# Optimization experiments

Measured on AMD Instinct MI355X. Metric: run time of the kernel, lower is better.

Reference implementation:

```python
import jax, jax.numpy as jnp
import numpy as np

B, IN_CH, HID, OUT_CH, GH, GW = 16, 64, 128, 64, 64, 64


def grid_edges(h, w):
    # torch_geometric.utils.grid: 8-neighborhood + self-loop, edge = (node, node+offset)
    idx = np.arange(h * w).reshape(h, w)
    rows, cols = [], []
    for dr in (-1, 0, 1):
        for dc in (-1, 0, 1):
            node = idx[max(0, -dr):h - max(0, dr), max(0, -dc):w - max(0, dc)]
            nb = idx[max(0, dr):h + min(0, dr) or None, max(0, dc):w + min(0, dc) or None]
            rows.append(node.ravel())
            cols.append(nb.ravel())
    return np.stack([np.concatenate(rows), np.concatenate(cols)])


def setup_inputs() -> dict:
    key = jax.random.key(0)
    ks = jax.random.split(key, 32)
    def rn(i, shape, scale=0.05):
        return jax.random.normal(ks[i], shape, dtype=jnp.float32) * scale
    e = grid_edges(GH, GW)                                   # (2, E)
    offs = (np.arange(B) * (GH * GW)).reshape(B, 1, 1)
    ei = (e[None] + offs).transpose(1, 0, 2).reshape(2, -1)  # (2, B*E) batched offsets
    return {
        "x": rn(0, (B, IN_CH, GH, GW), 1.0),
        "cW1": rn(1, (HID, IN_CH, 3, 3)), "cb1": rn(2, (HID,)),
        "cW2": rn(3, (IN_CH, HID, 3, 3)), "cb2": rn(4, (IN_CH,)),
        "q1W": rn(5, (HID, IN_CH)), "q1b": rn(6, (HID,)),
        "k1W": rn(7, (HID, IN_CH)), "k1b": rn(8, (HID,)),
        "v1W": rn(9, (HID, IN_CH)), "v1b": rn(10, (HID,)),
        "s1W": rn(11, (HID, IN_CH)), "s1b": rn(12, (HID,)),
        "q2W": rn(13, (IN_CH, HID)), "q2b": rn(14, (IN_CH,)),
        "k2W": rn(15, (IN_CH, HID)), "k2b": rn(16, (IN_CH,)),
        "v2W": rn(17, (IN_CH, HID)), "v2b": rn(18, (IN_CH,)),
        "s2W": rn(19, (IN_CH, HID)), "s2b": rn(20, (IN_CH,)),
        "fW1": rn(21, (HID, 2 * IN_CH, 3, 3)), "fb1": rn(22, (HID,)),
        "fW2": rn(23, (OUT_CH, HID, 3, 3)), "fb2": rn(24, (OUT_CH,)),
        "edge_index": jnp.asarray(ei, dtype=jnp.int32),
    }


def gelu(x):
    return jax.nn.gelu(x, approximate=False)


def sn_conv(x, W, b):
    # spectral_norm: power iteration on (O, I*k*k) matrix; u,v detached, grad through sigma
    O = W.shape[0]
    Wm = W.reshape(O, -1)
    u = jnp.ones((O,), W.dtype) / jnp.sqrt(jnp.asarray(O, W.dtype))
    for _ in range(3):
        v = Wm.T @ u
        v = v / (jnp.linalg.norm(v) + 1e-12)
        u = Wm @ v
        u = u / (jnp.linalg.norm(u) + 1e-12)
    u = jax.lax.stop_gradient(u)
    v = jax.lax.stop_gradient(v)
    sigma = u @ (Wm @ v)
    Wn = W / sigma
    xp = jnp.pad(x, ((0, 0), (0, 0), (1, 1), (1, 1)), mode='edge')  # replicate padding
    y = jax.lax.conv_general_dilated(xp, Wn, (1, 1), 'VALID',
                                     dimension_numbers=('NCHW', 'OIHW', 'NCHW'))
    return y + b[None, :, None, None]


def tconv(x, src, dst, N, heads, qW, qb, kW, kb, vW, vb, sW, sb):
    # PyG TransformerConv (concat=True, root_weight=True, no edge features)
    d = qW.shape[0] // heads
    q = (x @ qW.T + qb)[dst].reshape(-1, heads, d)
    k = (x @ kW.T + kb)[src].reshape(-1, heads, d)
    v = (x @ vW.T + vb)[src].reshape(-1, heads, d)
    alpha = (q * k).sum(-1) / jnp.sqrt(jnp.asarray(d, x.dtype))      # (E, heads)
    m = jax.ops.segment_max(alpha, dst, num_segments=N)               # scatter-softmax
    a = jnp.exp(alpha - m[dst])
    s = jax.ops.segment_sum(a, dst, num_segments=N)
    a = a / (s[dst] + 1e-16)
    out = jax.ops.segment_sum(a[:, :, None] * v, dst, num_segments=N)  # (N, heads, d)
    return out.reshape(N, heads * d) + x @ sW.T + sb


def reference(x, cW1, cb1, cW2, cb2, q1W, q1b, k1W, k1b, v1W, v1b, s1W, s1b,
              q2W, q2b, k2W, k2b, v2W, v2b, s2W, s2b, fW1, fb1, fW2, fb2, edge_index):
    Bb, C, Hc, Wc = x.shape
    N = Bb * Hc * Wc
    # CNN branch (DoubleConvBlock)
    x1 = gelu(sn_conv(gelu(sn_conv(x, cW1, cb1)), cW2, cb2))
    # GCN branch
    xf = x.transpose(0, 2, 3, 1).reshape(N, C)
    src, dst = edge_index[0], edge_index[1]
    h = gelu(tconv(xf, src, dst, N, 8, q1W, q1b, k1W, k1b, v1W, v1b, s1W, s1b))
    h = gelu(tconv(h, src, dst, N, 1, q2W, q2b, k2W, k2b, v2W, v2b, s2W, s2b))
    x2 = h.reshape(Bb, Hc, Wc, -1).transpose(0, 3, 1, 2)
    # Fusion
    xc = jnp.concatenate([x1, x2], axis=1)
    return gelu(sn_conv(gelu(sn_conv(xc, fW1, fb1)), fW2, fb2))
```

## Files before the change

kernel.cpp:

```cpp
#include <hip/hip_runtime.h>
#include <hip/hip_bf16.h>

typedef unsigned int  u32;
typedef unsigned short u16;
typedef __attribute__((ext_vector_type(8))) short bf16x8;
typedef __attribute__((ext_vector_type(4))) float f32x4;
typedef __attribute__((ext_vector_type(4))) u32 u32x4;

#define NPIX 65536

constexpr size_t SIG   = 0;
constexpr size_t B1OFF = 256;
constexpr size_t B2OFF = B1OFF + 2048;
constexpr size_t WC1   = B2OFF + 1024;
constexpr size_t WC2   = WC1 + 147456;
constexpr size_t WF1   = WC2 + 147456;
constexpr size_t WF2   = WF1 + 294912;
constexpr size_t WP1   = WF2 + 147456;
constexpr size_t WP2   = WP1 + 65536;
constexpr size_t XB    = WP2 + 65536;
constexpr size_t HBUF  = XB + 8388608;
constexpr size_t QKVS2 = HBUF + 16777216;
constexpr size_t XC    = QKVS2 + 33554432;
constexpr size_t QKVS1 = XC + 16777216;
constexpr size_t Y1    = QKVS1;
constexpr size_t TBUF  = QKVS1 + 16777216;
constexpr size_t GRAM  = QKVS1 + 67108864;

__device__ __forceinline__ float gelu_f(float v) {
    float xa = fabsf(v) * 0.70710678118654752f;
    float t  = __fdividef(1.0f, fmaf(0.3275911f, xa, 1.0f));
    float poly = t * fmaf(t, fmaf(t, fmaf(t, fmaf(t, 1.061405429f, -1.453152027f),
                   1.421413741f), -0.284496736f), 0.254829592f);
    float erfv = 1.0f - poly * __expf(-xa * xa);
    erfv = copysignf(erfv, v);
    return 0.5f * v * (1.0f + erfv);
}
__device__ __forceinline__ u16 f2bf(float f) {
    __hip_bfloat16 b = __float2bfloat16(f);
    return *reinterpret_cast<u16*>(&b);
}
__device__ __forceinline__ float blo(u32 u) {
    union { u32 i; float f; } x; x.i = u << 16; return x.f;
}
__device__ __forceinline__ float bhi(u32 u) {
    union { u32 i; float f; } x; x.i = u & 0xffff0000u; return x.f;
}
__device__ __forceinline__ u32 packbf(float a, float b) {
    return (u32)f2bf(a) | ((u32)f2bf(b) << 16);
}
__device__ __forceinline__ void g2l16(const void* g, void* l) {
    __builtin_amdgcn_global_load_lds(
        (const __attribute__((address_space(1))) u32*)g,
        (__attribute__((address_space(3))) u32*)l, 16, 0, 0);
}

__device__ float block_sum(float vv, float* red) {
    #pragma unroll
    for (int m = 1; m < 64; m <<= 1) vv += __shfl_xor(vv, m);
    int tid = threadIdx.x;
    __syncthreads();
    if ((tid & 63) == 0) red[tid >> 6] = vv;
    __syncthreads();
    return red[0] + red[1] + red[2] + red[3];
}

__global__ __launch_bounds__(256)
void gram_kernel(const float* __restrict__ cW1, const float* __restrict__ cW2,
                 const float* __restrict__ fW1, const float* __restrict__ fW2,
                 float* __restrict__ Gall) {
    int bid = blockIdx.x;
    const float* W; int O, K, wsel, tile;
    if (bid < 64)       { W = cW1; O = 128; K = 576;  wsel = 0; tile = bid; }
    else if (bid < 80)  { W = cW2; O = 64;  K = 1152; wsel = 1; tile = bid - 64; }
    else if (bid < 144) { W = fW1; O = 128; K = 1152; wsel = 2; tile = bid - 80; }
    else                { W = fW2; O = 64;  K = 1152; wsel = 3; tile = bid - 144; }
    int ntiles = O >> 4;
    int ti0 = (tile / ntiles) << 4, tj0 = (tile % ntiles) << 4;
    __shared__ float Wi[16][33], Wj[16][33];
    int tid = threadIdx.x;
    int ti = tid >> 4, tj = tid & 15;
    int r = tid >> 5, c = tid & 31;
    float acc = 0.f;
    for (int k0 = 0; k0 < K; k0 += 32) {
        Wi[r][c]     = W[(size_t)(ti0 + r) * K + k0 + c];
        Wi[r + 8][c] = W[(size_t)(ti0 + r + 8) * K + k0 + c];
        Wj[r][c]     = W[(size_t)(tj0 + r) * K + k0 + c];
        Wj[r + 8][c] = W[(size_t)(tj0 + r + 8) * K + k0 + c];
        __syncthreads();
        #pragma unroll
        for (int k = 0; k < 32; ++k)
            acc += Wi[ti][k] * Wj[tj][k];
        __syncthreads();
    }
    Gall[wsel * 16384 + (ti0 + ti) * 128 + (tj0 + tj)] = acc;
}

__global__ __launch_bounds__(256)
void power_kernel(const float* __restrict__ Gall, float* __restrict__ sig) {
    int wsel = blockIdx.x;
    const float* G = Gall + wsel * 16384;
    const int O = (wsel == 0 || wsel == 2) ? 128 : 64;
    __shared__ float u[128], t[128], red[4];
    int tid = threadIdx.x;
    if (tid < O) u[tid] = 1.0f / sqrtf((float)O);
    __syncthreads();
    for (int it = 0; it < 3; ++it) {
        if (tid < O) {
            float s = 0.f;
            const float4* gr = reinterpret_cast<const float4*>(G + (size_t)tid * 128);
            for (int j = 0; j < O / 4; ++j) {
                float4 g = gr[j];
                s += g.x * u[4*j] + g.y * u[4*j+1] + g.z * u[4*j+2] + g.w * u[4*j+3];
            }
            t[tid] = s;
        }
        __syncthreads();
        float loc = (tid < O) ? t[tid] * t[tid] : 0.f;
        float nt = sqrtf(block_sum(loc, red));
        if (it == 2) {
            float locd = (tid < O) ? u[tid] * t[tid] : 0.f;
            float dot = block_sum(locd, red);
            if (tid == 0) sig[wsel] = nt / sqrtf(dot + 1e-24f);
        } else {
            if (tid < O) u[tid] = t[tid] / (nt + 1e-12f);
            __syncthreads();
        }
    }
}

__global__ __launch_bounds__(256)
void prep_conv_w(const float* __restrict__ cW1, const float* __restrict__ cW2,
                 const float* __restrict__ fW1, const float* __restrict__ fW2,
                 const float* __restrict__ sig,
                 u16* wc1, u16* wc2, u16* wf1, u16* wf2) {
    int wsel = blockIdx.y;
    const float* src; u16* dst; int O, C;
    switch (wsel) {
        case 0:  src = cW1; dst = wc1; O = 128; C = 64;  break;
        case 1:  src = cW2; dst = wc2; O = 64;  C = 128; break;
        case 2:  src = fW1; dst = wf1; O = 128; C = 128; break;
        default: src = fW2; dst = wf2; O = 64;  C = 128; break;
    }
    int idx = blockIdx.x * 256 + threadIdx.x;
    if (idx >= O * C * 9) return;
    int o = idx / (C * 9);
    int rem = idx - o * (C * 9);
    int ci = rem / 9, tap = rem - ci * 9;
    float v = src[idx] / sig[wsel];
    dst[(size_t)o * (C * 9) + tap * C + ci] = f2bf(v);
}

__global__ __launch_bounds__(256)
void prep_proj(const float* q1W, const float* k1W, const float* v1W, const float* s1W,
               const float* q2W, const float* k2W, const float* v2W, const float* s2W,
               const float* q1b, const float* k1b, const float* v1b, const float* s1b,
               const float* q2b, const float* k2b, const float* v2b, const float* s2b,
               u16* wp1, u16* wp2, float* b1, float* b2) {
    const float* W1[4] = {q1W, k1W, v1W, s1W};
    const float* W2[4] = {q2W, k2W, v2W, s2W};
    const float* Bb1[4] = {q1b, k1b, v1b, s1b};
    const float* Bb2[4] = {q2b, k2b, v2b, s2b};
    int idx = blockIdx.x * 256 + threadIdx.x;
    if (idx < 32768) {
        int w = idx >> 13, r = idx & 8191;
        wp1[(size_t)w * 8192 + r] = f2bf(W1[w][r]);
    } else if (idx < 65536) {
        int j = idx - 32768; int w = j >> 13, r = j & 8191;
        wp2[(size_t)w * 8192 + r] = f2bf(W2[w][r]);
    } else if (idx < 66048) {
        int j = idx - 65536; int w = j >> 7; b1[j] = Bb1[w][j & 127];
    } else if (idx < 66304) {
        int j = idx - 66048; int w = j >> 6; b2[j] = Bb2[w][j & 63];
    }
}

__global__ __launch_bounds__(256)
void convert_x(const float* __restrict__ x, u16* __restrict__ xb) {
    __shared__ float tile[64][65];
    int b = blockIdx.x >> 6, y = blockIdx.x & 63;
    int tid = threadIdx.x;
    #pragma unroll
    for (int i = 0; i < 16; ++i) {
        int c = (tid >> 6) + i * 4;
        tile[c][tid & 63] = x[(((size_t)b * 64 + c) << 12) + (y << 6) + (tid & 63)];
    }
    __syncthreads();
    #pragma unroll
    for (int i = 0; i < 16; ++i) {
        int idx = tid + i * 256;
        int p = idx >> 6, c = idx & 63;
        xb[(((size_t)b << 12) + (y << 6) + p) * 64 + c] = f2bf(tile[c][p]);
    }
}

template<int TAPS, int CC, int BN, int OUTM>
__global__ __launch_bounds__(256)
void mm_kernel(const u16* __restrict__ A, const u16* __restrict__ Bw,
               const float* __restrict__ bias, void* __restrict__ Cout,
               int ostride, int ocol0, int do_gelu) {
    constexpr int K = CC * TAPS;
    constexpr int NSTEP = TAPS;
    constexpr int NCH = CC / 8;
    constexpr int NKS = CC / 32;
    constexpr int NF = BN / 32;
    constexpr int HN = BN / 2;
    constexpr int RSTEP = 256 / NCH;
    constexpr int ALD = 128 / RSTEP;
    constexpr int BLD = BN / RSTEP;
    __shared__ u16 Als[128 * CC];
    __shared__ u16 Bls[BN * CC];
    const int tid = threadIdx.x;
    const int w = tid >> 6;
    const int lane = tid & 63;
    const int m0 = blockIdx.x * 128;
    const int nt0 = blockIdx.y * BN;
    const int wm = w >> 1, wn = w & 1;

    const int srow = tid / NCH;
    const int sslot = tid % NCH;
    const int csrc = ((sslot ^ (srow & (NCH - 1))) << 3);
    const u16* Bbase = Bw + (size_t)(nt0 + srow) * K + csrc;

    int offA[NKS][4], offB[NKS][NF];
    #pragma unroll
    for (int ks = 0; ks < NKS; ++ks) {
        #pragma unroll
        for (int mf = 0; mf < 4; ++mf) {
            int R = wm * 64 + mf * 16 + (lane & 15);
            int slot = (ks * 4 + (lane >> 4)) ^ (R & (NCH - 1));
            offA[ks][mf] = R * CC + slot * 8;
        }
        #pragma unroll
        for (int nf = 0; nf < NF; ++nf) {
            int Rb = wn * HN + nf * 16 + (lane & 15);
            int slot = (ks * 4 + (lane >> 4)) ^ (Rb & (NCH - 1));
            offB[ks][nf] = Rb * CC + slot * 8;
        }
    }

    f32x4 acc[4][NF];
    #pragma unroll
    for (int i = 0; i < 4; ++i)
        #pragma unroll
        for (int j = 0; j < NF; ++j) {
            f32x4 z = {0.f, 0.f, 0.f, 0.f};
            acc[i][j] = z;
        }

    #pragma unroll
    for (int kt = 0; kt < NSTEP; ++kt) {
        const int kk = kt * CC;
        const int dy = (TAPS == 9) ? (kt / 3 - 1) : 0;
        const int dx = (TAPS == 9) ? (kt % 3 - 1) : 0;
        #pragma unroll
        for (int i = 0; i < ALD; ++i) {
            const int m = m0 + srow + i * RSTEP;
            const u16* ga;
            if constexpr (TAPS == 9) {
                int yy = ((m >> 6) & 63) + dy; yy = min(max(yy, 0), 63);
                int xx = (m & 63) + dx;        xx = min(max(xx, 0), 63);
                ga = A + (size_t)((m & ~4095) | (yy << 6) | xx) * CC + csrc;
            } else {
                ga = A + (size_t)m * CC + csrc;
            }
            g2l16(ga, &Als[(srow + i * RSTEP) * CC + sslot * 8]);
        }
        #pragma unroll
        for (int i = 0; i < BLD; ++i)
            g2l16(Bbase + (size_t)i * RSTEP * K + kk,
                  &Bls[(srow + i * RSTEP) * CC + sslot * 8]);

        __syncthreads();

        #pragma unroll
        for (int ks = 0; ks < NKS; ++ks) {
            bf16x8 af[4];
            #pragma unroll
            for (int mf = 0; mf < 4; ++mf)
                af[mf] = *reinterpret_cast<const bf16x8*>(&Als[offA[ks][mf]]);
            #pragma unroll
            for (int nf = 0; nf < NF; ++nf) {
                bf16x8 bfv = *reinterpret_cast<const bf16x8*>(&Bls[offB[ks][nf]]);
                #pragma unroll
                for (int mf = 0; mf < 4; ++mf)
                    acc[mf][nf] = __builtin_amdgcn_mfma_f32_16x16x32_bf16(
                        af[mf], bfv, acc[mf][nf], 0, 0, 0);
            }
        }
        if (kt + 1 < NSTEP) __syncthreads();
    }

    #pragma unroll
    for (int mf = 0; mf < 4; ++mf) {
        int mrow = m0 + wm * 64 + mf * 16 + (lane >> 4) * 4;
        #pragma unroll
        for (int nf = 0; nf < NF; ++nf) {
            int col = nt0 + wn * HN + nf * 16 + (lane & 15);
            float bv = bias[col];
            if (OUTM == 0) {
                u16* Co = (u16*)Cout;
                #pragma unroll
                for (int j = 0; j < 4; ++j) {
                    float v = acc[mf][nf][j] + bv;
                    if (do_gelu) v = gelu_f(v);
                    Co[(size_t)(mrow + j) * ostride + ocol0 + col] = f2bf(v);
                }
            } else {
                float* Co = (float*)Cout;
                int b = m0 >> 12;
                int pixb = (mrow & 4095);
                f32x4 vv;
                #pragma unroll
                for (int j = 0; j < 4; ++j)
                    vv[j] = gelu_f(acc[mf][nf][j] + bv);
                *reinterpret_cast<f32x4*>(&Co[((size_t)(b * 64 + col)) * 4096 + pixb]) = vv;
            }
        }
    }
}

__global__ __launch_bounds__(256)
void attn1_kernel(const u16* __restrict__ qkvs, u16* __restrict__ h) {
    const int tid = threadIdx.x;
    const int l16 = tid & 15;
    const int n = blockIdx.x * 16 + (tid >> 4);
    const int y = (n >> 6) & 63, x = n & 63;
    const u32* qk = (const u32*)qkvs;
    const int nbase = (n << 8) + l16 * 4;

    u32x4 qp = *(const u32x4*)(qk + nbase);
    float q[8];
    #pragma unroll
    for (int i = 0; i < 4; ++i) { q[2*i] = blo(qp[i]); q[2*i+1] = bhi(qp[i]); }

    float al[9];
    float mx = -1e30f;
    #pragma unroll
    for (int e = 0; e < 9; ++e) {
        const int dy = e / 3 - 1, dx = e % 3 - 1;
        const bool valid = (unsigned)(y + dy) < 64u && (unsigned)(x + dx) < 64u;
        const int off = valid ? ((dy * 64 + dx) << 8) : 0;
        u32x4 kp = *(const u32x4*)(qk + nbase + off + 64);
        float p = 0.f;
        #pragma unroll
        for (int i = 0; i < 4; ++i) {
            p = fmaf(q[2*i],   blo(kp[i]), p);
            p = fmaf(q[2*i+1], bhi(kp[i]), p);
        }
        p += __shfl_xor(p, 1);
        al[e] = valid ? p * 0.25f : -1e30f;
        mx = fmaxf(mx, al[e]);
    }
    float s = 0.f;
    #pragma unroll
    for (int e = 0; e < 9; ++e) { al[e] = __expf(al[e] - mx); s += al[e]; }

    float o[8] = {0.f, 0.f, 0.f, 0.f, 0.f, 0.f, 0.f, 0.f};
    #pragma unroll
    for (int e = 0; e < 9; ++e) {
        const int dy = e / 3 - 1, dx = e % 3 - 1;
        const bool valid = (unsigned)(y + dy) < 64u && (unsigned)(x + dx) < 64u;
        const int off = valid ? ((dy * 64 + dx) << 8) : 0;
        u32x4 vp = *(const u32x4*)(qk + nbase + off + 128);
        const float a = al[e];
        #pragma unroll
        for (int i = 0; i < 4; ++i) {
            o[2*i]   = fmaf(a, blo(vp[i]), o[2*i]);
            o[2*i+1] = fmaf(a, bhi(vp[i]), o[2*i+1]);
        }
    }
    const float r = __fdividef(1.0f, s + 1e-16f);
    u32x4 sp = *(const u32x4*)(qk + nbase + 192);
    u32x4 res;
    #pragma unroll
    for (int i = 0; i < 4; ++i) {
        float h0 = gelu_f(fmaf(o[2*i],   r, blo(sp[i])));
        float h1 = gelu_f(fmaf(o[2*i+1], r, bhi(sp[i])));
        res[i] = packbf(h0, h1);
    }
    *(u32x4*)((u32*)h + (n << 6) + l16 * 4) = res;
}

__global__ __launch_bounds__(256)
void attn2_kernel(const u16* __restrict__ qkvs, u16* __restrict__ xc) {
    const int tid = threadIdx.x;
    const int l8 = tid & 7;
    const int n = blockIdx.x * 32 + (tid >> 3);
    const int y = (n >> 6) & 63, x = n & 63;
    const u32* qk = (const u32*)qkvs;
    const int nbase = (n << 7) + l8 * 4;

    u32x4 qp = *(const u32x4*)(qk + nbase);
    float q[8];
    #pragma unroll
    for (int i = 0; i < 4; ++i) { q[2*i] = blo(qp[i]); q[2*i+1] = bhi(qp[i]); }

    float al[9];
    float mx = -1e30f;
    #pragma unroll
    for (int e = 0; e < 9; ++e) {
        const int dy = e / 3 - 1, dx = e % 3 - 1;
        const bool valid = (unsigned)(y + dy) < 64u && (unsigned)(x + dx) < 64u;
        const int off = valid ? ((dy * 64 + dx) << 7) : 0;
        u32x4 kp = *(const u32x4*)(qk + nbase + off + 32);
        float p = 0.f;
        #pragma unroll
        for (int i = 0; i < 4; ++i) {
            p = fmaf(q[2*i],   blo(kp[i]), p);
            p = fmaf(q[2*i+1], bhi(kp[i]), p);
        }
        p += __shfl_xor(p, 1);
        p += __shfl_xor(p, 2);
        p += __shfl_xor(p, 4);
        al[e] = valid ? p * 0.125f : -1e30f;
        mx = fmaxf(mx, al[e]);
    }
    float s = 0.f;
    #pragma unroll
    for (int e = 0; e < 9; ++e) { al[e] = __expf(al[e] - mx); s += al[e]; }

    float o[8] = {0.f, 0.f, 0.f, 0.f, 0.f, 0.f, 0.f, 0.f};
    #pragma unroll
    for (int e = 0; e < 9; ++e) {
        const int dy = e / 3 - 1, dx = e % 3 - 1;
        const bool valid = (unsigned)(y + dy) < 64u && (unsigned)(x + dx) < 64u;
        const int off = valid ? ((dy * 64 + dx) << 7) : 0;
        u32x4 vp = *(const u32x4*)(qk + nbase + off + 64);
        const float a = al[e];
        #pragma unroll
        for (int i = 0; i < 4; ++i) {
            o[2*i]   = fmaf(a, blo(vp[i]), o[2*i]);
            o[2*i+1] = fmaf(a, bhi(vp[i]), o[2*i+1]);
        }
    }
    const float r = __fdividef(1.0f, s + 1e-16f);
    u32x4 sp = *(const u32x4*)(qk + nbase + 96);
    u32x4 res;
    #pragma unroll
    for (int i = 0; i < 4; ++i) {
        float h0 = gelu_f(fmaf(o[2*i],   r, blo(sp[i])));
        float h1 = gelu_f(fmaf(o[2*i+1], r, bhi(sp[i])));
        res[i] = packbf(h0, h1);
    }
    *(u32x4*)((u32*)xc + (n << 6) + 32 + l8 * 4) = res;
}

extern "C" void kernel_launch(void* const* d_in, const int* in_sizes, int n_in,
                              void* d_out, int out_size, void* d_ws, size_t ws_size,
                              hipStream_t stream) {
    const float* x   = (const float*)d_in[0];
    const float* cW1 = (const float*)d_in[1];
    const float* cb1 = (const float*)d_in[2];
    const float* cW2 = (const float*)d_in[3];
    const float* cb2 = (const float*)d_in[4];
    const float* q1W = (const float*)d_in[5];
    const float* q1b = (const float*)d_in[6];
    const float* k1W = (const float*)d_in[7];
    const float* k1b = (const float*)d_in[8];
    const float* v1W = (const float*)d_in[9];
    const float* v1b = (const float*)d_in[10];
    const float* s1W = (const float*)d_in[11];
    const float* s1b = (const float*)d_in[12];
    const float* q2W = (const float*)d_in[13];
    const float* q2b = (const float*)d_in[14];
    const float* k2W = (const float*)d_in[15];
    const float* k2b = (const float*)d_in[16];
    const float* v2W = (const float*)d_in[17];
    const float* v2b = (const float*)d_in[18];
    const float* s2W = (const float*)d_in[19];
    const float* s2b = (const float*)d_in[20];
    const float* fW1 = (const float*)d_in[21];
    const float* fb1 = (const float*)d_in[22];
    const float* fW2 = (const float*)d_in[23];
    const float* fb2 = (const float*)d_in[24];

    char* ws = (char*)d_ws;
    float* sig  = (float*)(ws + SIG);
    float* b1   = (float*)(ws + B1OFF);
    float* b2   = (float*)(ws + B2OFF);
    u16* wc1    = (u16*)(ws + WC1);
    u16* wc2    = (u16*)(ws + WC2);
    u16* wf1    = (u16*)(ws + WF1);
    u16* wf2    = (u16*)(ws + WF2);
    u16* wp1    = (u16*)(ws + WP1);
    u16* wp2    = (u16*)(ws + WP2);
    u16* xb     = (u16*)(ws + XB);
    u16* hbuf   = (u16*)(ws + HBUF);
    u16* qkvs2  = (u16*)(ws + QKVS2);
    u16* xc     = (u16*)(ws + XC);
    u16* qkvs1  = (u16*)(ws + QKVS1);
    u16* y1     = (u16*)(ws + Y1);
    u16* tbuf   = (u16*)(ws + TBUF);
    float* gram = (float*)(ws + GRAM);
    float* out  = (float*)d_out;

    gram_kernel<<<160, 256, 0, stream>>>(cW1, cW2, fW1, fW2, gram);
    power_kernel<<<4, 256, 0, stream>>>(gram, sig);
    prep_conv_w<<<dim3(576, 4), 256, 0, stream>>>(cW1, cW2, fW1, fW2, sig,
                                                  wc1, wc2, wf1, wf2);
    prep_proj<<<260, 256, 0, stream>>>(q1W, k1W, v1W, s1W, q2W, k2W, v2W, s2W,
                                       q1b, k1b, v1b, s1b, q2b, k2b, v2b, s2b,
                                       wp1, wp2, b1, b2);
    convert_x<<<1024, 256, 0, stream>>>(x, xb);

    mm_kernel<1, 64, 128, 0><<<dim3(512, 4), 256, 0, stream>>>(
        xb, wp1, b1, qkvs1, 512, 0, 0);
    attn1_kernel<<<NPIX / 16, 256, 0, stream>>>(qkvs1, hbuf);
    mm_kernel<1, 128, 128, 0><<<dim3(512, 2), 256, 0, stream>>>(
        hbuf, wp2, b2, qkvs2, 256, 0, 0);
    attn2_kernel<<<NPIX / 32, 256, 0, stream>>>(qkvs2, xc);

    mm_kernel<9, 64, 128, 0><<<dim3(512, 1), 256, 0, stream>>>(
        xb, wc1, cb1, y1, 128, 0, 1);
    mm_kernel<9, 128, 64, 0><<<dim3(512, 1), 256, 0, stream>>>(
        y1, wc2, cb2, xc, 128, 0, 1);
    mm_kernel<9, 128, 128, 0><<<dim3(512, 1), 256, 0, stream>>>(
        xc, wf1, fb1, tbuf, 128, 0, 1);
    mm_kernel<9, 128, 64, 1><<<dim3(512, 1), 256, 0, stream>>>(
        tbuf, wf2, fb2, out, 0, 0, 1);
}
```

Before: 210.0 us.

## Add halo-tiled implicit-GEMM conv kernel with triple-buffered weight pipeline

```diff
diff --git a/kernel.cpp b/kernel.cpp
--- a/kernel.cpp
+++ b/kernel.cpp
@@ -53,6 +53,10 @@
     __builtin_amdgcn_global_load_lds(
         (const __attribute__((address_space(1))) u32*)g,
         (__attribute__((address_space(3))) u32*)l, 16, 0, 0);
+}
+template<int N>
+__device__ __forceinline__ void waitvm() {
+    asm volatile("s_waitcnt vmcnt(%0)" :: "n"(N) : "memory");
 }
 
 __device__ float block_sum(float vv, float* red) {
@@ -194,6 +198,143 @@
     }
 }
 
+template<int CCF, int NHALF, int BN, int OUTM>
+__global__ __launch_bounds__(512)
+void conv_kernel(const u16* __restrict__ A, const u16* __restrict__ Bw,
+                 const float* __restrict__ bias, void* __restrict__ Cout,
+                 int ostride, int ocol0, int do_gelu) {
+    constexpr int KFULL = CCF * 9;
+    constexpr int NF = BN / 32;
+    constexpr int HB = BN / 2;
+    constexpr int LPS = BN / 64;
+    constexpr int W = 72;
+    constexpr int NLR = 9;
+    __shared__ u16 Ah[6 * W * 64];
+    __shared__ u16 Bls[3][BN * 64];
+
+    const int tid = threadIdx.x;
+    const int w = tid >> 6;
+    const int lane = tid & 63;
+    const int wm = w >> 1, wn = w & 1;
+    const int img = blockIdx.x >> 4;
+    const int y0 = (blockIdx.x & 15) << 2;
+    const int lr = lane & 15, lg = lane >> 4;
+
+    const int cg8 = (((tid & 7) ^ ((tid >> 3) & 7)) << 3);
+    const int brow = tid >> 3;
+
+    int offB[2][NF];
+    #pragma unroll
+    for (int ks = 0; ks < 2; ++ks)
+        #pragma unroll
+        for (int nf = 0; nf < NF; ++nf) {
+            int Rb = wn * HB + nf * 16 + lr;
+            int cl = ks * 4 + lg;
+            offB[ks][nf] = Rb * 64 + ((cl ^ (Rb & 7)) << 3);
+        }
+
+    f32x4 acc[4][NF];
+    #pragma unroll
+    for (int i = 0; i < 4; ++i)
+        #pragma unroll
+        for (int j = 0; j < NF; ++j) {
+            f32x4 z = {0.f, 0.f, 0.f, 0.f};
+            acc[i][j] = z;
+        }
+
+    for (int h = 0; h < NHALF; ++h) {
+        __syncthreads();
+        {
+            const int cch = lane & 7;
+            const int cof = lane >> 3;
+            for (int L = w; L < 6 * NLR; L += 8) {
+                int row = L / NLR, cb = (L - row * NLR) * 8;
+                int c = cb + cof;
+                int yy = min(max(y0 + row - 1, 0), 63);
+                int xx = min(max(c - 1, 0), 63);
+                const u16* g = A + (size_t)((img << 12) + (yy << 6) + xx) * CCF
+                                 + h * 64 + ((cch ^ (c & 7)) << 3);
+                g2l16(g, &Ah[(row * W + cb) * 64]);
+            }
+        }
+        auto stageB = [&](int t) {
+            const int buf = t % 3;
+            #pragma unroll
+            for (int i = 0; i < LPS; ++i) {
+                const u16* g = Bw + (size_t)(brow + i * 64) * KFULL
+                                 + t * CCF + h * 64 + cg8;
+                g2l16(g, &Bls[buf][(i * 64 + (w << 3)) * 64]);
+            }
+        };
+        stageB(0);
+        stageB(1);
+        waitvm<LPS>();
+        __builtin_amdgcn_s_barrier();
+        __builtin_amdgcn_sched_barrier(0);
+
+        #pragma unroll
+        for (int t = 0; t < 9; ++t) {
+            if (t + 2 < 9) stageB(t + 2);
+            __builtin_amdgcn_sched_barrier(0);
+            const int dy = t / 3 - 1, dx = t % 3 - 1;
+            const u16* Bb = &Bls[t % 3][0];
+            #pragma unroll
+            for (int ks = 0; ks < 2; ++ks) {
+                bf16x8 af[4];
+                #pragma unroll
+                for (int mf = 0; mf < 4; ++mf) {
+                    int col = mf * 16 + lr + dx + 1;
+                    int addr = ((wm + dy + 1) * W + col) * 64
+                             + (((ks * 4 + lg) ^ (col & 7)) << 3);
+                    af[mf] = *reinterpret_cast<const bf16x8*>(&Ah[addr]);
+                }
+                #pragma unroll
+                for (int nf = 0; nf < NF; ++nf) {
+                    bf16x8 bv = *reinterpret_cast<const bf16x8*>(Bb + offB[ks][nf]);
+                    #pragma unroll
+                    for (int mf = 0; mf < 4; ++mf)
+                        acc[mf][nf] = __builtin_amdgcn_mfma_f32_16x16x32_bf16(
+                            af[mf], bv, acc[mf][nf], 0, 0, 0);
+                }
+            }
+            __builtin_amdgcn_sched_barrier(0);
+            if (t < 8) {
+                if (t + 2 < 9) waitvm<LPS>();
+                else           waitvm<0>();
+                __builtin_amdgcn_s_barrier();
+            }
+        }
+    }
+
+    #pragma unroll
+    for (int mf = 0; mf < 4; ++mf) {
+        int x = mf * 16 + lg * 4;
+        #pragma unroll
+        for (int nf = 0; nf < NF; ++nf) {
+            int ch = wn * HB + nf * 16 + lr;
+            float bv = bias[ch];
+            if (OUTM == 0) {
+                u16* Co = (u16*)Cout;
+                int n = (img << 12) + ((y0 + wm) << 6) + x;
+                #pragma unroll
+                for (int j = 0; j < 4; ++j) {
+                    float v = acc[mf][nf][j] + bv;
+                    if (do_gelu) v = gelu_f(v);
+                    Co[(size_t)(n + j) * ostride + ocol0 + ch] = f2bf(v);
+                }
+            } else {
+                float* Co = (float*)Cout;
+                f32x4 vv;
+                #pragma unroll
+                for (int j = 0; j < 4; ++j)
+                    vv[j] = gelu_f(acc[mf][nf][j] + bv);
+                *reinterpret_cast<f32x4*>(
+                    &Co[((size_t)((img << 6) + ch) << 12) + ((y0 + wm) << 6) + x]) = vv;
+            }
+        }
+    }
+}
+
 template<int TAPS, int CC, int BN, int OUTM>
 __global__ __launch_bounds__(256)
 void mm_kernel(const u16* __restrict__ A, const u16* __restrict__ Bw,
@@ -251,20 +392,11 @@
     #pragma unroll
     for (int kt = 0; kt < NSTEP; ++kt) {
         const int kk = kt * CC;
-        const int dy = (TAPS == 9) ? (kt / 3 - 1) : 0;
-        const int dx = (TAPS == 9) ? (kt % 3 - 1) : 0;
         #pragma unroll
         for (int i = 0; i < ALD; ++i) {
             const int m = m0 + srow + i * RSTEP;
-            const u16* ga;
-            if constexpr (TAPS == 9) {
-                int yy = ((m >> 6) & 63) + dy; yy = min(max(yy, 0), 63);
-                int xx = (m & 63) + dx;        xx = min(max(xx, 0), 63);
-                ga = A + (size_t)((m & ~4095) | (yy << 6) | xx) * CC + csrc;
-            } else {
-                ga = A + (size_t)m * CC + csrc;
-            }
-            g2l16(ga, &Als[(srow + i * RSTEP) * CC + sslot * 8]);
+            g2l16(A + (size_t)m * CC + kk + csrc,
+                  &Als[(srow + i * RSTEP) * CC + sslot * 8]);
         }
         #pragma unroll
         for (int i = 0; i < BLD; ++i)
@@ -298,23 +430,12 @@
         for (int nf = 0; nf < NF; ++nf) {
             int col = nt0 + wn * HN + nf * 16 + (lane & 15);
             float bv = bias[col];
-            if (OUTM == 0) {
-                u16* Co = (u16*)Cout;
-                #pragma unroll
-                for (int j = 0; j < 4; ++j) {
-                    float v = acc[mf][nf][j] + bv;
-                    if (do_gelu) v = gelu_f(v);
-                    Co[(size_t)(mrow + j) * ostride + ocol0 + col] = f2bf(v);
-                }
-            } else {
-                float* Co = (float*)Cout;
-                int b = m0 >> 12;
-                int pixb = (mrow & 4095);
-                f32x4 vv;
-                #pragma unroll
-                for (int j = 0; j < 4; ++j)
-                    vv[j] = gelu_f(acc[mf][nf][j] + bv);
-                *reinterpret_cast<f32x4*>(&Co[((size_t)(b * 64 + col)) * 4096 + pixb]) = vv;
+            u16* Co = (u16*)Cout;
+            #pragma unroll
+            for (int j = 0; j < 4; ++j) {
+                float v = acc[mf][nf][j] + bv;
+                if (do_gelu) v = gelu_f(v);
+                Co[(size_t)(mrow + j) * ostride + ocol0 + col] = f2bf(v);
             }
         }
     }
@@ -511,12 +632,8 @@
         hbuf, wp2, b2, qkvs2, 256, 0, 0);
     attn2_kernel<<<NPIX / 32, 256, 0, stream>>>(qkvs2, xc);
 
-    mm_kernel<9, 64, 128, 0><<<dim3(512, 1), 256, 0, stream>>>(
-        xb, wc1, cb1, y1, 128, 0, 1);
-    mm_kernel<9, 128, 64, 0><<<dim3(512, 1), 256, 0, stream>>>(
-        y1, wc2, cb2, xc, 128, 0, 1);
-    mm_kernel<9, 128, 128, 0><<<dim3(512, 1), 256, 0, stream>>>(
-        xc, wf1, fb1, tbuf, 128, 0, 1);
-    mm_kernel<9, 128, 64, 1><<<dim3(512, 1), 256, 0, stream>>>(
-        tbuf, wf2, fb2, out, 0, 0, 1);
-}
+    conv_kernel<64, 1, 128, 0><<<256, 512, 0, stream>>>(xb, wc1, cb1, y1, 128, 0, 1);
+    conv_kernel<128, 2, 64, 0><<<256, 512, 0, stream>>>(y1, wc2, cb2, xc, 128, 0, 1);
+    conv_kernel<128, 2, 128, 0><<<256, 512, 0, stream>>>(xc, wf1, fb1, tbuf, 128, 0, 1);
+    conv_kernel<128, 2, 64, 1><<<256, 512, 0, stream>>>(tbuf, wf2, fb2, out, 0, 0, 1);
+}
```

After: 211.3 us. No clear change (+0.6%).

## Merge independent stages into horizontally fused kernels to cut launch count

Applied to the files above, without the earlier changes.

```diff
diff --git a/kernel.cpp b/kernel.cpp
--- a/kernel.cpp
+++ b/kernel.cpp
@@ -23,7 +23,6 @@
 constexpr size_t QKVS2 = HBUF + 16777216;
 constexpr size_t XC    = QKVS2 + 33554432;
 constexpr size_t QKVS1 = XC + 16777216;
-constexpr size_t Y1    = QKVS1;
 constexpr size_t TBUF  = QKVS1 + 16777216;
 constexpr size_t GRAM  = QKVS1 + 67108864;
 
@@ -65,11 +64,10 @@
     return red[0] + red[1] + red[2] + red[3];
 }
 
-__global__ __launch_bounds__(256)
-void gram_kernel(const float* __restrict__ cW1, const float* __restrict__ cW2,
-                 const float* __restrict__ fW1, const float* __restrict__ fW2,
-                 float* __restrict__ Gall) {
-    int bid = blockIdx.x;
+
+__device__ void gram_body(int bid, char* smem,
+                          const float* cW1, const float* cW2,
+                          const float* fW1, const float* fW2, float* Gall) {
     const float* W; int O, K, wsel, tile;
     if (bid < 64)       { W = cW1; O = 128; K = 576;  wsel = 0; tile = bid; }
     else if (bid < 80)  { W = cW2; O = 64;  K = 1152; wsel = 1; tile = bid - 64; }
@@ -77,7 +75,8 @@
     else                { W = fW2; O = 64;  K = 1152; wsel = 3; tile = bid - 144; }
     int ntiles = O >> 4;
     int ti0 = (tile / ntiles) << 4, tj0 = (tile % ntiles) << 4;
-    __shared__ float Wi[16][33], Wj[16][33];
+    float (*Wi)[33] = (float(*)[33])smem;
+    float (*Wj)[33] = (float(*)[33])(smem + 16 * 33 * 4);
     int tid = threadIdx.x;
     int ti = tid >> 4, tj = tid & 15;
     int r = tid >> 5, c = tid & 31;
@@ -96,63 +95,27 @@
     Gall[wsel * 16384 + (ti0 + ti) * 128 + (tj0 + tj)] = acc;
 }
 
-__global__ __launch_bounds__(256)
-void power_kernel(const float* __restrict__ Gall, float* __restrict__ sig) {
-    int wsel = blockIdx.x;
-    const float* G = Gall + wsel * 16384;
-    const int O = (wsel == 0 || wsel == 2) ? 128 : 64;
-    __shared__ float u[128], t[128], red[4];
+__device__ void convert_body(int bid, char* smem,
+                             const float* __restrict__ x, u16* __restrict__ xb) {
+    float (*tile)[65] = (float(*)[65])smem;
+    int b = bid >> 6, y = bid & 63;
     int tid = threadIdx.x;
-    if (tid < O) u[tid] = 1.0f / sqrtf((float)O);
+    #pragma unroll
+    for (int i = 0; i < 16; ++i) {
+        int c = (tid >> 6) + i * 4;
+        tile[c][tid & 63] = x[(((size_t)b * 64 + c) << 12) + (y << 6) + (tid & 63)];
+    }
     __syncthreads();
-    for (int it = 0; it < 3; ++it) {
-        if (tid < O) {
-            float s = 0.f;
-            const float4* gr = reinterpret_cast<const float4*>(G + (size_t)tid * 128);
-            for (int j = 0; j < O / 4; ++j) {
-                float4 g = gr[j];
-                s += g.x * u[4*j] + g.y * u[4*j+1] + g.z * u[4*j+2] + g.w * u[4*j+3];
-            }
-            t[tid] = s;
-        }
-        __syncthreads();
-        float loc = (tid < O) ? t[tid] * t[tid] : 0.f;
-        float nt = sqrtf(block_sum(loc, red));
-        if (it == 2) {
-            float locd = (tid < O) ? u[tid] * t[tid] : 0.f;
-            float dot = block_sum(locd, red);
-            if (tid == 0) sig[wsel] = nt / sqrtf(dot + 1e-24f);
-        } else {
-            if (tid < O) u[tid] = t[tid] / (nt + 1e-12f);
-            __syncthreads();
-        }
-    }
-}
-
-__global__ __launch_bounds__(256)
-void prep_conv_w(const float* __restrict__ cW1, const float* __restrict__ cW2,
-                 const float* __restrict__ fW1, const float* __restrict__ fW2,
-                 const float* __restrict__ sig,
-                 u16* wc1, u16* wc2, u16* wf1, u16* wf2) {
-    int wsel = blockIdx.y;
-    const float* src; u16* dst; int O, C;
-    switch (wsel) {
-        case 0:  src = cW1; dst = wc1; O = 128; C = 64;  break;
-        case 1:  src = cW2; dst = wc2; O = 64;  C = 128; break;
-        case 2:  src = fW1; dst = wf1; O = 128; C = 128; break;
-        default: src = fW2; dst = wf2; O = 64;  C = 128; break;
-    }
-    int idx = blockIdx.x * 256 + threadIdx.x;
-    if (idx >= O * C * 9) return;
-    int o = idx / (C * 9);
-    int rem = idx - o * (C * 9);
-    int ci = rem / 9, tap = rem - ci * 9;
-    float v = src[idx] / sig[wsel];
-    dst[(size_t)o * (C * 9) + tap * C + ci] = f2bf(v);
-}
-
-__global__ __launch_bounds__(256)
-void prep_proj(const float* q1W, const float* k1W, const float* v1W, const float* s1W,
+    #pragma unroll
+    for (int i = 0; i < 16; ++i) {
+        int idx = tid + i * 256;
+        int p = idx >> 6, c = idx & 63;
+        xb[(((size_t)b << 12) + (y << 6) + p) * 64 + c] = f2bf(tile[c][p]);
+    }
+}
+
+__device__ void prep_proj_body(int bid,
+               const float* q1W, const float* k1W, const float* v1W, const float* s1W,
                const float* q2W, const float* k2W, const float* v2W, const float* s2W,
                const float* q1b, const float* k1b, const float* v1b, const float* s1b,
                const float* q2b, const float* k2b, const float* v2b, const float* s2b,
@@ -161,7 +124,7 @@
     const float* W2[4] = {q2W, k2W, v2W, s2W};
     const float* Bb1[4] = {q1b, k1b, v1b, s1b};
     const float* Bb2[4] = {q2b, k2b, v2b, s2b};
-    int idx = blockIdx.x * 256 + threadIdx.x;
+    int idx = bid * 256 + threadIdx.x;
     if (idx < 32768) {
         int w = idx >> 13, r = idx & 8191;
         wp1[(size_t)w * 8192 + r] = f2bf(W1[w][r]);
@@ -175,28 +138,30 @@
     }
 }
 
-__global__ __launch_bounds__(256)
-void convert_x(const float* __restrict__ x, u16* __restrict__ xb) {
-    __shared__ float tile[64][65];
-    int b = blockIdx.x >> 6, y = blockIdx.x & 63;
-    int tid = threadIdx.x;
-    #pragma unroll
-    for (int i = 0; i < 16; ++i) {
-        int c = (tid >> 6) + i * 4;
-        tile[c][tid & 63] = x[(((size_t)b * 64 + c) << 12) + (y << 6) + (tid & 63)];
-    }
-    __syncthreads();
-    #pragma unroll
-    for (int i = 0; i < 16; ++i) {
-        int idx = tid + i * 256;
-        int p = idx >> 6, c = idx & 63;
-        xb[(((size_t)b << 12) + (y << 6) + p) * 64 + c] = f2bf(tile[c][p]);
-    }
+__device__ void prep_conv_w_body(int bx, int wsel,
+                 const float* __restrict__ cW1, const float* __restrict__ cW2,
+                 const float* __restrict__ fW1, const float* __restrict__ fW2,
+                 const float* __restrict__ sig,
+                 u16* wc1, u16* wc2, u16* wf1, u16* wf2) {
+    const float* src; u16* dst; int O, C;
+    switch (wsel) {
+        case 0:  src = cW1; dst = wc1; O = 128; C = 64;  break;
+        case 1:  src = cW2; dst = wc2; O = 64;  C = 128; break;
+        case 2:  src = fW1; dst = wf1; O = 128; C = 128; break;
+        default: src = fW2; dst = wf2; O = 64;  C = 128; break;
+    }
+    int idx = bx * 256 + threadIdx.x;
+    if (idx >= O * C * 9) return;
+    int o = idx / (C * 9);
+    int rem = idx - o * (C * 9);
+    int ci = rem / 9, tap = rem - ci * 9;
+    float v = src[idx] / sig[wsel];
+    dst[(size_t)o * (C * 9) + tap * C + ci] = f2bf(v);
 }
 
 template<int TAPS, int CC, int BN, int OUTM>
-__global__ __launch_bounds__(256)
-void mm_kernel(const u16* __restrict__ A, const u16* __restrict__ Bw,
+__device__ void mm_body(int bx, int by, char* smem,
+               const u16* __restrict__ A, const u16* __restrict__ Bw,
                const float* __restrict__ bias, void* __restrict__ Cout,
                int ostride, int ocol0, int do_gelu) {
     constexpr int K = CC * TAPS;
@@ -208,13 +173,13 @@
     constexpr int RSTEP = 256 / NCH;
     constexpr int ALD = 128 / RSTEP;
     constexpr int BLD = BN / RSTEP;
-    __shared__ u16 Als[128 * CC];
-    __shared__ u16 Bls[BN * CC];
+    u16* Als = (u16*)smem;
+    u16* Bls = (u16*)smem + 128 * CC;
     const int tid = threadIdx.x;
     const int w = tid >> 6;
     const int lane = tid & 63;
-    const int m0 = blockIdx.x * 128;
-    const int nt0 = blockIdx.y * BN;
+    const int m0 = bx * 128;
+    const int nt0 = by * BN;
     const int wm = w >> 1, wn = w & 1;
 
     const int srow = tid / NCH;
@@ -320,11 +285,11 @@
     }
 }
 
-__global__ __launch_bounds__(256)
-void attn1_kernel(const u16* __restrict__ qkvs, u16* __restrict__ h) {
+__device__ void attn1_body(int bid, const u16* __restrict__ qkvs,
+                           u16* __restrict__ h) {
     const int tid = threadIdx.x;
     const int l16 = tid & 15;
-    const int n = blockIdx.x * 16 + (tid >> 4);
+    const int n = bid * 16 + (tid >> 4);
     const int y = (n >> 6) & 63, x = n & 63;
     const u32* qk = (const u32*)qkvs;
     const int nbase = (n << 8) + l16 * 4;
@@ -380,6 +345,40 @@
         res[i] = packbf(h0, h1);
     }
     *(u32x4*)((u32*)h + (n << 6) + l16 * 4) = res;
+}
+
+
+__global__ __launch_bounds__(256)
+void power_kernel(const float* __restrict__ Gall, float* __restrict__ sig) {
+    int wsel = blockIdx.x;
+    const float* G = Gall + wsel * 16384;
+    const int O = (wsel == 0 || wsel == 2) ? 128 : 64;
+    __shared__ float u[128], t[128], red[4];
+    int tid = threadIdx.x;
+    if (tid < O) u[tid] = 1.0f / sqrtf((float)O);
+    __syncthreads();
+    for (int it = 0; it < 3; ++it) {
+        if (tid < O) {
+            float s = 0.f;
+            const float4* gr = reinterpret_cast<const float4*>(G + (size_t)tid * 128);
+            for (int j = 0; j < O / 4; ++j) {
+                float4 g = gr[j];
+                s += g.x * u[4*j] + g.y * u[4*j+1] + g.z * u[4*j+2] + g.w * u[4*j+3];
+            }
+            t[tid] = s;
+        }
+        __syncthreads();
+        float loc = (tid < O) ? t[tid] * t[tid] : 0.f;
+        float nt = sqrtf(block_sum(loc, red));
+        if (it == 2) {
+            float locd = (tid < O) ? u[tid] * t[tid] : 0.f;
+            float dot = block_sum(locd, red);
+            if (tid == 0) sig[wsel] = nt / sqrtf(dot + 1e-24f);
+        } else {
+            if (tid < O) u[tid] = t[tid] / (nt + 1e-12f);
+            __syncthreads();
+        }
+    }
 }
 
 __global__ __launch_bounds__(256)
@@ -444,6 +443,76 @@
         res[i] = packbf(h0, h1);
     }
     *(u32x4*)((u32*)xc + (n << 6) + 32 + l8 * 4) = res;
+}
+
+template<int TAPS, int CC, int BN, int OUTM>
+__global__ __launch_bounds__(256)
+void mm_kernel(const u16* __restrict__ A, const u16* __restrict__ Bw,
+               const float* __restrict__ bias, void* __restrict__ Cout,
+               int ostride, int ocol0, int do_gelu) {
+    __shared__ __align__(16) char smem[(128 * CC + BN * CC) * 2];
+    mm_body<TAPS, CC, BN, OUTM>(blockIdx.x, blockIdx.y, smem, A, Bw, bias, Cout,
+                                ostride, ocol0, do_gelu);
+}
+
+__global__ __launch_bounds__(256)
+void fuse_misc(const float* cW1, const float* cW2, const float* fW1,
+               const float* fW2, float* Gall,
+               const float* x, u16* xb,
+               const float* q1W, const float* k1W, const float* v1W, const float* s1W,
+               const float* q2W, const float* k2W, const float* v2W, const float* s2W,
+               const float* q1b, const float* k1b, const float* v1b, const float* s1b,
+               const float* q2b, const float* k2b, const float* v2b, const float* s2b,
+               u16* wp1, u16* wp2, float* b1, float* b2) {
+    __shared__ __align__(16) char smem[16640];
+    int bid = blockIdx.x;
+    if (bid < 1024)       convert_body(bid, smem, x, xb);
+    else if (bid < 1184)  gram_body(bid - 1024, smem, cW1, cW2, fW1, fW2, Gall);
+    else                  prep_proj_body(bid - 1184, q1W, k1W, v1W, s1W,
+                                         q2W, k2W, v2W, s2W, q1b, k1b, v1b, s1b,
+                                         q2b, k2b, v2b, s2b, wp1, wp2, b1, b2);
+}
+
+__global__ __launch_bounds__(256)
+void fuse_p1_w(const u16* xb, const u16* wp1, const float* b1, u16* qkvs1,
+               const float* cW1, const float* cW2, const float* fW1,
+               const float* fW2, const float* sig,
+               u16* wc1, u16* wc2, u16* wf1, u16* wf2) {
+    __shared__ __align__(16) char smem[(128 * 64 + 128 * 64) * 2];
+    int bid = blockIdx.x;
+    if (bid < 2048)
+        mm_body<1, 64, 128, 0>(bid & 511, bid >> 9, smem, xb, wp1, b1,
+                               (void*)qkvs1, 512, 0, 0);
+    else {
+        int wk = bid - 2048;
+        prep_conv_w_body(wk % 576, wk / 576, cW1, cW2, fW1, fW2, sig,
+                         wc1, wc2, wf1, wf2);
+    }
+}
+
+__global__ __launch_bounds__(256)
+void fuse_c1_a1(const u16* xb, const u16* wc1, const float* cb1, u16* y1,
+                const u16* qkvs1, u16* hbuf) {
+    __shared__ __align__(16) char smem[(128 * 64 + 128 * 64) * 2];
+    int bid = blockIdx.x;
+    if (bid < 512)
+        mm_body<9, 64, 128, 0>(bid, 0, smem, xb, wc1, cb1, (void*)y1, 128, 0, 1);
+    else
+        attn1_body(bid - 512, qkvs1, hbuf);
+}
+
+__global__ __launch_bounds__(256)
+void fuse_c2_p2(const u16* y1, const u16* wc2, const float* cb2, u16* xc,
+                const u16* hbuf, const u16* wp2, const float* b2, u16* qkvs2) {
+    __shared__ __align__(16) char smem[(128 * 128 + 128 * 128) * 2];
+    int bid = blockIdx.x;
+    if (bid < 512)
+        mm_body<9, 128, 64, 0>(bid, 0, smem, y1, wc2, cb2, (void*)xc, 128, 0, 1);
+    else {
+        int wk = bid - 512;
+        mm_body<1, 128, 128, 0>(wk & 511, wk >> 9, smem, hbuf, wp2, b2,
+                                (void*)qkvs2, 256, 0, 0);
+    }
 }
 
 extern "C" void kernel_launch(void* const* d_in, const int* in_sizes, int n_in,
@@ -490,31 +559,20 @@
     u16* qkvs2  = (u16*)(ws + QKVS2);
     u16* xc     = (u16*)(ws + XC);
     u16* qkvs1  = (u16*)(ws + QKVS1);
-    u16* y1     = (u16*)(ws + Y1);
     u16* tbuf   = (u16*)(ws + TBUF);
     float* gram = (float*)(ws + GRAM);
     float* out  = (float*)d_out;
-
-    gram_kernel<<<160, 256, 0, stream>>>(cW1, cW2, fW1, fW2, gram);
+    u16* y1     = (u16*)d_out;
+
+    fuse_misc<<<1444, 256, 0, stream>>>(cW1, cW2, fW1, fW2, gram, x, xb,
+        q1W, k1W, v1W, s1W, q2W, k2W, v2W, s2W,
+        q1b, k1b, v1b, s1b, q2b, k2b, v2b, s2b, wp1, wp2, b1, b2);
     power_kernel<<<4, 256, 0, stream>>>(gram, sig);
-    prep_conv_w<<<dim3(576, 4), 256, 0, stream>>>(cW1, cW2, fW1, fW2, sig,
-                                                  wc1, wc2, wf1, wf2);
-    prep_proj<<<260, 256, 0, stream>>>(q1W, k1W, v1W, s1W, q2W, k2W, v2W, s2W,
-                                       q1b, k1b, v1b, s1b, q2b, k2b, v2b, s2b,
-                                       wp1, wp2, b1, b2);
-    convert_x<<<1024, 256, 0, stream>>>(x, xb);
-
-    mm_kernel<1, 64, 128, 0><<<dim3(512, 4), 256, 0, stream>>>(
-        xb, wp1, b1, qkvs1, 512, 0, 0);
-    attn1_kernel<<<NPIX / 16, 256, 0, stream>>>(qkvs1, hbuf);
-    mm_kernel<1, 128, 128, 0><<<dim3(512, 2), 256, 0, stream>>>(
-        hbuf, wp2, b2, qkvs2, 256, 0, 0);
+    fuse_p1_w<<<4352, 256, 0, stream>>>(xb, wp1, b1, qkvs1,
+        cW1, cW2, fW1, fW2, sig, wc1, wc2, wf1, wf2);
+    fuse_c1_a1<<<4608, 256, 0, stream>>>(xb, wc1, cb1, y1, qkvs1, hbuf);
+    fuse_c2_p2<<<1536, 256, 0, stream>>>(y1, wc2, cb2, xc, hbuf, wp2, b2, qkvs2);
     attn2_kernel<<<NPIX / 32, 256, 0, stream>>>(qkvs2, xc);
-
-    mm_kernel<9, 64, 128, 0><<<dim3(512, 1), 256, 0, stream>>>(
-        xb, wc1, cb1, y1, 128, 0, 1);
-    mm_kernel<9, 128, 64, 0><<<dim3(512, 1), 256, 0, stream>>>(
-        y1, wc2, cb2, xc, 128, 0, 1);
     mm_kernel<9, 128, 128, 0><<<dim3(512, 1), 256, 0, stream>>>(
         xc, wf1, fb1, tbuf, 128, 0, 1);
     mm_kernel<9, 128, 64, 1><<<dim3(512, 1), 256, 0, stream>>>(
```

Result: faster. 193.2 us (-8.0%).
